# Optimization experiments

Measured on AMD Instinct MI355X. Metric: run time of the kernel, lower is better.

The kernel has to match this reference:

```python
import jax, jax.numpy as jnp
import numpy as np

QMIN_ACT, QMAX_ACT = -128.0, 127.0   # int8 activation range
QMIN_W, QMAX_W = -8, 7               # int4 weight range (values already in-range)


def setup_inputs() -> dict:
    key = jax.random.key(0)
    k1, k2, k3, k4 = jax.random.split(key, 4)
    B, S, K, O, G = 4, 2048, 4096, 11008, 128
    x = jax.random.normal(k1, (B, S, K), dtype=jnp.float32)
    # int4 weights stored as int8 in [-8, 7]
    weight = jax.random.randint(k2, (O, K), -8, 8, dtype=jnp.int32).astype(jnp.int8)
    # per-group scales (positive, realistic magnitude) and integer zero points
    scales = jax.random.uniform(k3, (K // G, O, 1), minval=1e-3, maxval=2e-2, dtype=jnp.float32)
    zeros = jnp.round(jax.random.uniform(k4, (K // G, O, 1), minval=-4.0, maxval=4.0, dtype=jnp.float32))
    scales_and_zeros = jnp.concatenate([scales, zeros], axis=-1)  # [K//G, O, 2]
    return {"x": x, "weight": weight, "scales_and_zeros": scales_and_zeros, "group_size": G}


def reference(x, weight, scales_and_zeros, group_size):
    # --- per-token int8 dynamic quant/dequant of activations (symmetric, zp=0) ---
    amax = jnp.max(jnp.abs(x), axis=-1, keepdims=True)            # [B,S,1]
    a_scales = jnp.maximum(amax, 1e-5) / QMAX_ACT
    q = jnp.clip(jnp.round(x / a_scales), QMIN_ACT, QMAX_ACT)
    x_dq = q * a_scales                                           # fake-quantized activations

    # --- per-channel-group int4 weight dequant ---
    O, K = weight.shape
    G = group_size
    sz = jnp.transpose(scales_and_zeros, (1, 0, 2))               # [O, K//G, 2]
    w_scales = sz[..., 0:1]                                       # [O, K//G, 1]
    w_zeros = sz[..., 1:2]
    w = weight.reshape(O, K // G, G).astype(jnp.float32)
    w_dq = ((w - w_zeros) * w_scales).reshape(O, K)               # [O, K]

    # --- dense linear ---
    out = jnp.einsum("bsk,ok->bso", x_dq, w_dq)                   # [B,S,O]
    return out
```

## Files before the change

kernel.cpp:

```cpp
#include <hip/hip_runtime.h>
#include <stdint.h>

#define MDIM 8192
#define NDIM 11008
#define KDIM 4096
#define GRP  128
#define NBLK (NDIM / 128)
#define MBLK (MDIM / 128)
#define PANEL 16

typedef __attribute__((ext_vector_type(8))) __bf16 bf16x8;
typedef __attribute__((ext_vector_type(4))) float f32x4;
typedef __attribute__((ext_vector_type(4))) unsigned short u16x4;

static __device__ __forceinline__ unsigned short f2bf(float f) {
    union { float f; unsigned int u; } c; c.f = f;
    unsigned int u = c.u;
    u += 0x7fffu + ((u >> 16) & 1u);
    return (unsigned short)(u >> 16);
}

__global__ __launch_bounds__(256) void quant_x_kernel(const float* __restrict__ x,
                                                      unsigned short* __restrict__ xq) {
    __shared__ float red[256];
    const int row = blockIdx.x;
    const int tid = threadIdx.x;
    const float* xr = x + (size_t)row * KDIM;

    f32x4 v[4];
    float amax = 0.f;
#pragma unroll
    for (int i = 0; i < 4; ++i) {
        v[i] = *(const f32x4*)(xr + 4 * (tid + 256 * i));
        amax = fmaxf(amax, fmaxf(fmaxf(fabsf(v[i].x), fabsf(v[i].y)),
                                 fmaxf(fabsf(v[i].z), fabsf(v[i].w))));
    }
    red[tid] = amax;
    __syncthreads();
    for (int s = 128; s > 0; s >>= 1) {
        if (tid < s) red[tid] = fmaxf(red[tid], red[tid + s]);
        __syncthreads();
    }
    const float scale = fmaxf(red[0], 1e-5f) / 127.0f;

#pragma unroll
    for (int i = 0; i < 4; ++i) {
        u16x4 ov;
        float q;
        q = fminf(fmaxf(rintf(v[i].x / scale), -128.f), 127.f); ov.x = f2bf(q * scale);
        q = fminf(fmaxf(rintf(v[i].y / scale), -128.f), 127.f); ov.y = f2bf(q * scale);
        q = fminf(fmaxf(rintf(v[i].z / scale), -128.f), 127.f); ov.z = f2bf(q * scale);
        q = fminf(fmaxf(rintf(v[i].w / scale), -128.f), 127.f); ov.w = f2bf(q * scale);
        *(u16x4*)(xq + (size_t)row * KDIM + 4 * (tid + 256 * i)) = ov;
    }
}

__global__ __launch_bounds__(256) void dequant_w_kernel(const int* __restrict__ w,
                                                        const float* __restrict__ sz,
                                                        unsigned short* __restrict__ wq) {
    const int idx = blockIdx.x * 256 + threadIdx.x;
    const int kc = idx & (KDIM / 4 - 1);
    const int o  = idx >> 10;
    const int k0 = kc << 2;
    const int g  = k0 >> 7;
    const float2 szv = *(const float2*)(sz + ((size_t)g * NDIM + o) * 2);
    const float s = szv.x, z = szv.y;
    const int4 wv = *(const int4*)(w + (size_t)o * KDIM + k0);
    u16x4 ov;
    ov.x = f2bf(((float)wv.x - z) * s);
    ov.y = f2bf(((float)wv.y - z) * s);
    ov.z = f2bf(((float)wv.z - z) * s);
    ov.w = f2bf(((float)wv.w - z) * s);
    *(u16x4*)(wq + (size_t)o * KDIM + k0) = ov;
}

__global__ __launch_bounds__(256) void gemm_bt_kernel(const unsigned short* __restrict__ A,
                                                      const unsigned short* __restrict__ B,
                                                      float* __restrict__ C) {
    __shared__ unsigned short As[128 * 32];
    __shared__ unsigned short Bs[128 * 32];

    const int tid  = threadIdx.x;
    const int lane = tid & 63;
    const int wave = tid >> 6;
    const int quad = lane >> 4;
    const int l16  = lane & 15;

    const int lid   = blockIdx.y * NBLK + blockIdx.x;
    const int pb    = PANEL * NBLK;
    const int panel = lid / pb;
    const int rem   = lid - panel * pb;
    const int n_idx = rem >> 4;
    const int m_idx = rem & (PANEL - 1);
    const int bm = (panel * PANEL + m_idx) * 128;
    const int bn = n_idx * 128;

    const int wm = (wave >> 1) * 64;
    const int wn = (wave & 1) * 64;

    f32x4 acc[4][4];
#pragma unroll
    for (int i = 0; i < 4; ++i)
#pragma unroll
        for (int j = 0; j < 4; ++j) acc[i][j] = (f32x4){0.f, 0.f, 0.f, 0.f};

    const int rlo = tid >> 2;
    const int kof = ((tid & 3) ^ ((rlo >> 1) & 3)) * 8;
    const unsigned short* gA0 = A + (size_t)(bm + rlo) * KDIM + kof;
    const unsigned short* gA1 = A + (size_t)(bm + 64 + rlo) * KDIM + kof;
    const unsigned short* gB0 = B + (size_t)(bn + rlo) * KDIM + kof;
    const unsigned short* gB1 = B + (size_t)(bn + 64 + rlo) * KDIM + kof;
    unsigned short* lA0 = As + tid * 8;
    unsigned short* lA1 = As + (tid + 256) * 8;
    unsigned short* lB0 = Bs + tid * 8;
    unsigned short* lB1 = Bs + (tid + 256) * 8;

    const int sw = (quad ^ ((l16 >> 1) & 3)) * 8;

    for (int k0 = 0; k0 < KDIM; k0 += 32) {
        __syncthreads();
        __builtin_amdgcn_global_load_lds((const __attribute__((address_space(1))) void*)(gA0 + k0),
                                         (__attribute__((address_space(3))) void*)lA0, 16, 0, 0);
        __builtin_amdgcn_global_load_lds((const __attribute__((address_space(1))) void*)(gA1 + k0),
                                         (__attribute__((address_space(3))) void*)lA1, 16, 0, 0);
        __builtin_amdgcn_global_load_lds((const __attribute__((address_space(1))) void*)(gB0 + k0),
                                         (__attribute__((address_space(3))) void*)lB0, 16, 0, 0);
        __builtin_amdgcn_global_load_lds((const __attribute__((address_space(1))) void*)(gB1 + k0),
                                         (__attribute__((address_space(3))) void*)lB1, 16, 0, 0);
        __syncthreads();

        bf16x8 af[4], bfr[4];
#pragma unroll
        for (int i = 0; i < 4; ++i)
            af[i] = *(const bf16x8*)(As + (wm + i * 16 + l16) * 32 + sw);
#pragma unroll
        for (int j = 0; j < 4; ++j)
            bfr[j] = *(const bf16x8*)(Bs + (wn + j * 16 + l16) * 32 + sw);

#pragma unroll
        for (int i = 0; i < 4; ++i)
#pragma unroll
            for (int j = 0; j < 4; ++j)
                acc[i][j] = __builtin_amdgcn_mfma_f32_16x16x32_bf16(af[i], bfr[j], acc[i][j], 0, 0, 0);
    }

#pragma unroll
    for (int i = 0; i < 4; ++i) {
        const int mbase = bm + wm + i * 16 + quad * 4;
#pragma unroll
        for (int r = 0; r < 4; ++r) {
            float* crow = C + (size_t)(mbase + r) * NDIM + bn + wn + l16;
#pragma unroll
            for (int j = 0; j < 4; ++j) crow[j * 16] = acc[i][j][r];
        }
    }
}

extern "C" void kernel_launch(void* const* d_in, const int* in_sizes, int n_in,
                              void* d_out, int out_size, void* d_ws, size_t ws_size,
                              hipStream_t stream) {
    const float* x  = (const float*)d_in[0];
    const int*   w  = (const int*)d_in[1];
    const float* sz = (const float*)d_in[2];
    float* out = (float*)d_out;

    unsigned short* xq = (unsigned short*)d_ws;
    unsigned short* wq = (unsigned short*)((char*)d_ws + (size_t)MDIM * KDIM * 2);

    quant_x_kernel<<<MDIM, 256, 0, stream>>>(x, xq);
    dequant_w_kernel<<<(NDIM * KDIM / 4) / 256, 256, 0, stream>>>(w, sz, wq);
    gemm_bt_kernel<<<dim3(NBLK, MBLK), 256, 0, stream>>>(xq, wq, out);
}
```

Baseline: 1.543 ms.

## Rewrite GEMM as 256x256 tile, 8-wave, double-buffered pipelined kernel with XCD swizzle

Replaces the 128x128x32 single-buffered GEMM with a 256x256x64 tile computed by 512 threads, using double-buffered LDS and global-to-LDS prefetch interleaved with MFMA phases. Waitcnt and barriers are placed by hand, with setprio around MFMA bursts. Blocks are remapped so neighbouring tiles share an XCD for L2 reuse. This targets exposed memory latency and per-barrier stalls in the old loop, at the cost of higher register and LDS use (one block per CU) and fragile manual synchronisation.

```diff
diff --git a/kernel.cpp b/kernel.cpp
--- a/kernel.cpp
+++ b/kernel.cpp
@@ -5,9 +5,15 @@
 #define NDIM 11008
 #define KDIM 4096
 #define GRP  128
-#define NBLK (NDIM / 128)
-#define MBLK (MDIM / 128)
-#define PANEL 16
+
+#define BM 256
+#define BN 256
+#define BK 64
+#define NT   (KDIM / BK)
+#define MT   (MDIM / BM)
+#define NTLS (NDIM / BN)
+#define NWG  (MT * NTLS)
+#define CPX  (NWG / 8)
 
 typedef __attribute__((ext_vector_type(8))) __bf16 bf16x8;
 typedef __attribute__((ext_vector_type(4))) float f32x4;
@@ -74,84 +80,150 @@
     *(u16x4*)(wq + (size_t)o * KDIM + k0) = ov;
 }
 
-__global__ __launch_bounds__(256) void gemm_bt_kernel(const unsigned short* __restrict__ A,
-                                                      const unsigned short* __restrict__ B,
-                                                      float* __restrict__ C) {
-    __shared__ unsigned short As[128 * 32];
-    __shared__ unsigned short Bs[128 * 32];
+#define GLD(g, l)                                                                   \
+    __builtin_amdgcn_global_load_lds((const __attribute__((address_space(1))) void*)(g), \
+                                     (__attribute__((address_space(3))) void*)(l), 16, 0, 0)
+
+#define LDS_A(ks, row) (*(const bf16x8*)(Ab + (ks) * 8192 + (row) * 32 + sw))
+#define LDS_B(ks, row) (*(const bf16x8*)(Bb + (ks) * 8192 + (row) * 32 + sw))
+
+#define MFMA16(MH)                                                                  \
+    _Pragma("unroll") for (int i = 0; i < 4; ++i)                                   \
+        _Pragma("unroll") for (int j = 0; j < 4; ++j)                               \
+            acc[(MH) * 4 + i][j] =                                                  \
+                __builtin_amdgcn_mfma_f32_16x16x32_bf16(af[i], bv[j], acc[(MH) * 4 + i][j], 0, 0, 0);
+
+__global__ __launch_bounds__(512, 1) void gemm_bt_kernel(const unsigned short* __restrict__ A,
+                                                         const unsigned short* __restrict__ B,
+                                                         float* __restrict__ C) {
+    __shared__ unsigned short As_f[32768];
+    __shared__ unsigned short Bs_f[32768];
 
     const int tid  = threadIdx.x;
     const int lane = tid & 63;
     const int wave = tid >> 6;
     const int quad = lane >> 4;
     const int l16  = lane & 15;
-
-    const int lid   = blockIdx.y * NBLK + blockIdx.x;
-    const int pb    = PANEL * NBLK;
-    const int panel = lid / pb;
-    const int rem   = lid - panel * pb;
-    const int n_idx = rem >> 4;
-    const int m_idx = rem & (PANEL - 1);
-    const int bm = (panel * PANEL + m_idx) * 128;
-    const int bn = n_idx * 128;
-
-    const int wm = (wave >> 1) * 64;
-    const int wn = (wave & 1) * 64;
-
-    f32x4 acc[4][4];
-#pragma unroll
-    for (int i = 0; i < 4; ++i)
+    const int wm   = (wave >> 2) * 128;
+    const int wn   = (wave & 3) * 64;
+
+    const int bid  = blockIdx.x;
+    const int swzb = (bid & 7) * CPX + (bid >> 3);
+    const int bm   = (swzb & (MT - 1)) * BM;
+    const int bn   = (swzb / MT) * BN;
+
+    const int trow = tid >> 2;
+    const int kswz = (((tid & 3) ^ ((tid >> 3) & 3)) << 3);
+    const unsigned short* pA0 = A + (size_t)(bm + trow) * KDIM + kswz;
+    const unsigned short* pA1 = pA0 + (size_t)128 * KDIM;
+    const unsigned short* pB0 = B + (size_t)(bn + trow) * KDIM + kswz;
+    const unsigned short* pB1 = pB0 + (size_t)128 * KDIM;
+    unsigned short* dA = As_f + tid * 8;
+    unsigned short* dB = Bs_f + tid * 8;
+
+    const int sw = ((quad ^ ((l16 >> 1) & 3)) << 3);
+
+    f32x4 acc[8][4];
+#pragma unroll
+    for (int i = 0; i < 8; ++i)
 #pragma unroll
         for (int j = 0; j < 4; ++j) acc[i][j] = (f32x4){0.f, 0.f, 0.f, 0.f};
 
-    const int rlo = tid >> 2;
-    const int kof = ((tid & 3) ^ ((rlo >> 1) & 3)) * 8;
-    const unsigned short* gA0 = A + (size_t)(bm + rlo) * KDIM + kof;
-    const unsigned short* gA1 = A + (size_t)(bm + 64 + rlo) * KDIM + kof;
-    const unsigned short* gB0 = B + (size_t)(bn + rlo) * KDIM + kof;
-    const unsigned short* gB1 = B + (size_t)(bn + 64 + rlo) * KDIM + kof;
-    unsigned short* lA0 = As + tid * 8;
-    unsigned short* lA1 = As + (tid + 256) * 8;
-    unsigned short* lB0 = Bs + tid * 8;
-    unsigned short* lB1 = Bs + (tid + 256) * 8;
-
-    const int sw = (quad ^ ((l16 >> 1) & 3)) * 8;
-
-    for (int k0 = 0; k0 < KDIM; k0 += 32) {
-        __syncthreads();
-        __builtin_amdgcn_global_load_lds((const __attribute__((address_space(1))) void*)(gA0 + k0),
-                                         (__attribute__((address_space(3))) void*)lA0, 16, 0, 0);
-        __builtin_amdgcn_global_load_lds((const __attribute__((address_space(1))) void*)(gA1 + k0),
-                                         (__attribute__((address_space(3))) void*)lA1, 16, 0, 0);
-        __builtin_amdgcn_global_load_lds((const __attribute__((address_space(1))) void*)(gB0 + k0),
-                                         (__attribute__((address_space(3))) void*)lB0, 16, 0, 0);
-        __builtin_amdgcn_global_load_lds((const __attribute__((address_space(1))) void*)(gB1 + k0),
-                                         (__attribute__((address_space(3))) void*)lB1, 16, 0, 0);
-        __syncthreads();
-
-        bf16x8 af[4], bfr[4];
-#pragma unroll
-        for (int i = 0; i < 4; ++i)
-            af[i] = *(const bf16x8*)(As + (wm + i * 16 + l16) * 32 + sw);
-#pragma unroll
-        for (int j = 0; j < 4; ++j)
-            bfr[j] = *(const bf16x8*)(Bs + (wn + j * 16 + l16) * 32 + sw);
-
-#pragma unroll
-        for (int i = 0; i < 4; ++i)
-#pragma unroll
-            for (int j = 0; j < 4; ++j)
-                acc[i][j] = __builtin_amdgcn_mfma_f32_16x16x32_bf16(af[i], bfr[j], acc[i][j], 0, 0, 0);
-    }
-
-#pragma unroll
-    for (int i = 0; i < 4; ++i) {
-        const int mbase = bm + wm + i * 16 + quad * 4;
+    GLD(pA0,      dA);          GLD(pA1,      dA + 4096);
+    GLD(pB0,      dB);          GLD(pB1,      dB + 4096);
+    GLD(pA0 + 32, dA + 8192);   GLD(pA1 + 32, dA + 12288);
+    GLD(pB0 + 32, dB + 8192);   GLD(pB1 + 32, dB + 12288);
+    GLD(pA0 + 64, dA + 16384);  GLD(pA1 + 64, dA + 20480);
+    GLD(pB0 + 64, dB + 16384);  GLD(pB1 + 64, dB + 20480);
+    asm volatile("s_waitcnt vmcnt(8)" ::: "memory");
+    __builtin_amdgcn_s_barrier();
+
+    int buf = 0;
+    for (int t = 0; t < NT; ++t) {
+        const unsigned short* Ab = As_f + buf * 16384;
+        const unsigned short* Bb = Bs_f + buf * 16384;
+        unsigned short* dAn = dA + (buf ^ 1) * 16384;
+        unsigned short* dBn = dB + (buf ^ 1) * 16384;
+        unsigned short* dAc = dA + buf * 16384;
+        unsigned short* dBc = dB + buf * 16384;
+
+        bf16x8 af[4], bv[4];
+
+#pragma unroll
+        for (int i = 0; i < 4; ++i) af[i] = LDS_A(0, wm + i * 16 + l16);
+#pragma unroll
+        for (int j = 0; j < 4; ++j) bv[j] = LDS_B(0, wn + j * 16 + l16);
+        if (t < NT - 1) {
+            GLD(pA0 + (t + 1) * 64 + 32, dAn + 8192);
+            GLD(pA1 + (t + 1) * 64 + 32, dAn + 12288);
+        }
+        __builtin_amdgcn_s_barrier();
+        asm volatile("s_waitcnt lgkmcnt(0)" ::: "memory");
+        __builtin_amdgcn_sched_barrier(0);
+        __builtin_amdgcn_s_setprio(1);
+        MFMA16(0);
+        __builtin_amdgcn_s_setprio(0);
+        __builtin_amdgcn_s_barrier();
+
+#pragma unroll
+        for (int i = 0; i < 4; ++i) af[i] = LDS_A(0, wm + 64 + i * 16 + l16);
+        if (t < NT - 1) {
+            GLD(pB0 + (t + 1) * 64 + 32, dBn + 8192);
+            GLD(pB1 + (t + 1) * 64 + 32, dBn + 12288);
+        }
+        __builtin_amdgcn_s_barrier();
+        asm volatile("s_waitcnt lgkmcnt(0)" ::: "memory");
+        __builtin_amdgcn_sched_barrier(0);
+        __builtin_amdgcn_s_setprio(1);
+        MFMA16(1);
+        __builtin_amdgcn_s_setprio(0);
+        if (t < NT - 1) asm volatile("s_waitcnt vmcnt(8)" ::: "memory");
+        else            asm volatile("s_waitcnt vmcnt(0)" ::: "memory");
+        __builtin_amdgcn_s_barrier();
+
+#pragma unroll
+        for (int i = 0; i < 4; ++i) af[i] = LDS_A(1, wm + i * 16 + l16);
+#pragma unroll
+        for (int j = 0; j < 4; ++j) bv[j] = LDS_B(1, wn + j * 16 + l16);
+        if (t < NT - 2) {
+            GLD(pA0 + (t + 2) * 64, dAc);
+            GLD(pA1 + (t + 2) * 64, dAc + 4096);
+        }
+        __builtin_amdgcn_s_barrier();
+        asm volatile("s_waitcnt lgkmcnt(0)" ::: "memory");
+        __builtin_amdgcn_sched_barrier(0);
+        __builtin_amdgcn_s_setprio(1);
+        MFMA16(0);
+        __builtin_amdgcn_s_setprio(0);
+        __builtin_amdgcn_s_barrier();
+
+#pragma unroll
+        for (int i = 0; i < 4; ++i) af[i] = LDS_A(1, wm + 64 + i * 16 + l16);
+        if (t < NT - 2) {
+            GLD(pB0 + (t + 2) * 64, dBc);
+            GLD(pB1 + (t + 2) * 64, dBc + 4096);
+        }
+        __builtin_amdgcn_s_barrier();
+        asm volatile("s_waitcnt lgkmcnt(0)" ::: "memory");
+        __builtin_amdgcn_sched_barrier(0);
+        __builtin_amdgcn_s_setprio(1);
+        MFMA16(1);
+        __builtin_amdgcn_s_setprio(0);
+        if (t < NT - 2) asm volatile("s_waitcnt vmcnt(8)" ::: "memory");
+        else            asm volatile("s_waitcnt vmcnt(0)" ::: "memory");
+        __builtin_amdgcn_s_barrier();
+
+        buf ^= 1;
+    }
+
+#pragma unroll
+    for (int mi = 0; mi < 8; ++mi) {
+        const int gm = bm + wm + mi * 16 + quad * 4;
 #pragma unroll
         for (int r = 0; r < 4; ++r) {
-            float* crow = C + (size_t)(mbase + r) * NDIM + bn + wn + l16;
-#pragma unroll
-            for (int j = 0; j < 4; ++j) crow[j * 16] = acc[i][j][r];
+            float* crow = C + (size_t)(gm + r) * NDIM + bn + wn + l16;
+#pragma unroll
+            for (int j = 0; j < 4; ++j) crow[j * 16] = acc[mi][j][r];
         }
     }
 }
@@ -169,5 +241,5 @@
 
     quant_x_kernel<<<MDIM, 256, 0, stream>>>(x, xq);
     dequant_w_kernel<<<(NDIM * KDIM / 4) / 256, 256, 0, stream>>>(w, sz, wq);
-    gemm_bt_kernel<<<dim3(NBLK, MBLK), 256, 0, stream>>>(xq, wq, out);
-}
+    gemm_bt_kernel<<<NWG, 512, 0, stream>>>(xq, wq, out);
+}
```

Result: slower. 1.728 ms (+12.0%).
